# Optimization experiments

Hardware: AMD Instinct MI355X
Metric: run time of the kernel (lower is better)

The kernel has to match this reference:

```python
import jax, jax.numpy as jnp
import numpy as np

SLOPE_IN = 0.01  # F.leaky_relu default in the wrapper
SLOPE = 0.2      # DGCNN convention inside EdgeConv blocks
K = 40           # num_points -> k nearest neighbors
LOW = 16         # lowest_size: decoder starting grid
DOM = 128        # domain_size: output grid


def lrelu(x, s):
    return jnp.where(x >= 0, x, s * x)


def conv2d(x, w, b, stride, pad):
    y = jax.lax.conv_general_dilated(x, w, stride, pad,
                                     dimension_numbers=('NCHW', 'OIHW', 'NCHW'))
    return y + b[None, :, None, None]


def knn_idx(x, k):
    # x: (B,C,N) -> (B,N,k) indices of k nearest neighbors (incl. self)
    xx = jnp.sum(x * x, axis=1)                   # (B,N)
    inner = jnp.einsum('bcn,bcm->bnm', x, x)      # (B,N,N)
    neg_d = 2.0 * inner - xx[:, :, None] - xx[:, None, :]
    _, idx = jax.lax.top_k(neg_d, k)
    return idx


def graph_feature(x, idx):
    # x: (B,C,N), idx: (B,N,k) -> (B,2C,N,k): concat(neighbor - center, center)
    nbr = jax.vmap(lambda xf, i: xf[:, i])(x, idx)   # (B,C,N,k)
    ctr = jnp.broadcast_to(x[..., None], nbr.shape)
    return jnp.concatenate([nbr - ctr, ctr], axis=1)


def edge_conv(x, w, b, k):
    # dynamic graph: recompute kNN on current features
    idx = knn_idx(x, k)
    f = graph_feature(x, idx)                                      # (B,2C,N,k)
    h = jnp.einsum('oc,bcnk->bonk', w, f) + b[None, :, None, None]
    return jnp.max(lrelu(h, SLOPE), axis=-1)                       # (B,O,N)


def up2(x):
    return jnp.repeat(jnp.repeat(x, 2, axis=2), 2, axis=3)


def setup_inputs() -> dict:
    key = jax.random.key(0)
    ks = jax.random.split(key, 16)

    def w(k, shape, fan_in):
        return jax.random.normal(k, shape, jnp.float32) / np.float32(np.sqrt(fan_in))

    z = lambda n: jnp.zeros((n,), jnp.float32)
    return {
        'x':  jax.random.normal(ks[0], (2, 10, 2048), jnp.float32),
        'Wc': w(ks[1], (1, 1, 5, 3), 15),      'bc': z(1),
        'W1': w(ks[2], (64, 4), 4),            'b1': z(64),
        'W2': w(ks[3], (64, 128), 128),        'b2': z(64),
        'W3': w(ks[4], (128, 128), 128),       'b3': z(128),
        'W4': w(ks[5], (256, 256), 256),       'b4': z(256),
        'W5': w(ks[6], (1024, 512), 512),      'b5': z(1024),
        'Wfc': w(ks[7], (LOW * LOW * 64, 1024), 1024), 'bfc': z(LOW * LOW * 64),
        'Wd1': w(ks[8], (32, 64, 3, 3), 64 * 9),  'bd1': z(32),
        'Wd2': w(ks[9], (16, 32, 3, 3), 32 * 9),  'bd2': z(16),
        'Wd3': w(ks[10], (1, 16, 3, 3), 16 * 9),  'bd3': z(1),
    }


def reference(x, Wc, bc, W1, b1, W2, b2, W3, b3, W4, b4, W5, b5,
              Wfc, bfc, Wd1, bd1, Wd2, bd2, Wd3, bd3):
    # prefix: conv2d (5,3)/(5,1) + leaky_relu -> (B,1,2,N) -> point coords (B,2,N)
    h = conv2d(x[:, None, :, :], Wc, bc, (5, 1), ((0, 0), (1, 1)))
    h = lrelu(h, SLOPE_IN)[:, 0]                         # (B,2,N)
    # dynamic-graph EdgeConv stack
    x1 = edge_conv(h, W1, b1, K)                         # (B,64,N)
    x2 = edge_conv(x1, W2, b2, K)                        # (B,64,N)
    x3 = edge_conv(x2, W3, b3, K)                        # (B,128,N)
    x4 = edge_conv(x3, W4, b4, K)                        # (B,256,N)
    cat = jnp.concatenate([x1, x2, x3, x4], axis=1)      # (B,512,N)
    g = lrelu(jnp.einsum('oc,bcn->bon', W5, cat) + b5[None, :, None], SLOPE)
    g = jnp.max(g, axis=-1)                              # (B,1024) global feature
    d = lrelu(g @ Wfc.T + bfc, SLOPE).reshape(-1, 64, LOW, LOW)
    d = lrelu(conv2d(up2(d), Wd1, bd1, (1, 1), ((1, 1), (1, 1))), SLOPE)
    d = lrelu(conv2d(up2(d), Wd2, bd2, (1, 1), ((1, 1), (1, 1))), SLOPE)
    d = conv2d(up2(d), Wd3, bd3, (1, 1), ((1, 1), (1, 1)))
    return d
```

## Files before the change

kernel.cpp:

```cpp
#include <hip/hip_runtime.h>
#include <hip/hip_bf16.h>

#define N_PTS 2048
#define BATCH 2
#define KNN 40

typedef __attribute__((ext_vector_type(8))) short bf16x8;
typedef __attribute__((ext_vector_type(16))) float f32x16;

__device__ __forceinline__ float lrelu(float v, float s) {
    return v >= 0.f ? v : s * v;
}

__global__ void prefix_kernel(const float* __restrict__ x, const float* __restrict__ Wc,
                              const float* __restrict__ bc, float* __restrict__ H) {
    int t = blockIdx.x * 256 + threadIdx.x;
    if (t >= BATCH * N_PTS) return;
    int b = t >> 11, n = t & 2047;
    #pragma unroll
    for (int oh = 0; oh < 2; ++oh) {
        float acc = bc[0];
        #pragma unroll
        for (int kh = 0; kh < 5; ++kh) {
            const float* xr = x + ((size_t)b * 10 + oh * 5 + kh) * N_PTS;
            #pragma unroll
            for (int kw = 0; kw < 3; ++kw) {
                int nn = n + kw - 1;
                if (nn >= 0 && nn < N_PTS) acc += xr[nn] * Wc[kh * 3 + kw];
            }
        }
        H[(size_t)t * 2 + oh] = lrelu(acc, 0.01f);
    }
}

__global__ void xx_kernel(const float* __restrict__ X, int S, long bsX, int C,
                          float* __restrict__ XX) {
    int t = blockIdx.x * 256 + threadIdx.x;
    if (t >= BATCH * N_PTS) return;
    int b = t >> 11, n = t & 2047;
    const float* row = X + (size_t)b * bsX + (size_t)n * S;
    float s = 0.f;
    for (int c4 = 0; c4 < C; c4 += 4) {
        float4 q = *(const float4*)(row + c4);
        s += q.x * q.x;
        s += q.y * q.y;
        s += q.z * q.z;
        s += q.w * q.w;
    }
    XX[t] = s;
}

__global__ __launch_bounds__(256) void gram_small_kernel(const float* __restrict__ X, long bsX,
                                                         long nstride,
                                                         float* __restrict__ negd) {
    __shared__ float AsT[2][68];
    __shared__ float BsT[2][68];
    __shared__ float xxr[64];
    __shared__ float xxc[64];
    int bz = blockIdx.z;
    const float* Xb = X + (size_t)bz * bsX;
    float* nd = negd + (size_t)bz * nstride;
    int tid = threadIdx.x;
    int r0 = blockIdx.y * 64, c0 = blockIdx.x * 64;
    int ty = tid >> 4, tx = tid & 15;
    if (tid < 128) {
        int r = tid >> 1, c = tid & 1;
        AsT[c][r] = Xb[(size_t)(r0 + r) * 2 + c];
        BsT[c][r] = Xb[(size_t)(c0 + r) * 2 + c];
        int v = (tid < 64) ? (r0 + tid) : (c0 + tid - 64);
        float x0 = Xb[(size_t)v * 2], x1 = Xb[(size_t)v * 2 + 1];
        float s = 0.f;
        s += x0 * x0;
        s += x1 * x1;
        if (tid < 64) xxr[tid] = s; else xxc[tid - 64] = s;
    }
    __syncthreads();
    float acc[4][4] = {};
    #pragma unroll
    for (int k = 0; k < 2; ++k) {
        float4 a = *(const float4*)&AsT[k][ty * 4];
        float4 b = *(const float4*)&BsT[k][tx * 4];
        #pragma unroll
        for (int i = 0; i < 4; ++i)
            #pragma unroll
            for (int j = 0; j < 4; ++j)
                acc[i][j] += (&a.x)[i] * (&b.x)[j];
    }
    #pragma unroll
    for (int i = 0; i < 4; ++i) {
        int r = r0 + ty * 4 + i;
        float xr = xxr[ty * 4 + i];
        #pragma unroll
        for (int j = 0; j < 4; ++j) {
            int c = c0 + tx * 4 + j;
            nd[(size_t)r * N_PTS + c] = 2.0f * acc[i][j] - xr - xxc[tx * 4 + j];
        }
    }
}

template<int C>
__global__ void cvt_split_strided_kernel(const float* __restrict__ src, int S,
                                         short* __restrict__ hi, short* __restrict__ lo,
                                         int totalRows) {
    int t = blockIdx.x * 256 + threadIdx.x;
    constexpr int perRow = C / 4;
    int row = t / perRow, c4 = (t % perRow) * 4;
    if (row >= totalRows) return;
    float4 v = *(const float4*)(src + (size_t)row * S + c4);
    short4 h, l;
    #pragma unroll
    for (int j = 0; j < 4; ++j) {
        float xv = (&v.x)[j];
        __hip_bfloat16 hb = __float2bfloat16(xv);
        float hf = __bfloat162float(hb);
        __hip_bfloat16 lb = __float2bfloat16(xv - hf);
        (&h.x)[j] = *reinterpret_cast<short*>(&hb);
        (&l.x)[j] = *reinterpret_cast<short*>(&lb);
    }
    *(short4*)(hi + (size_t)row * C + c4) = h;
    *(short4*)(lo + (size_t)row * C + c4) = l;
}

template<int C, int STAGE>
__global__ __launch_bounds__(256) void gram_mfma_kernel(
        const short* __restrict__ Xh, const short* __restrict__ Xl, long bsX,
        const float* __restrict__ xx, long xxstride,
        float* __restrict__ negd, long nstride) {
    constexpr int NCH = C / 16;
    __shared__ float xr_s[128];
    __shared__ float xc_s[128];
    int bz = blockIdx.z;
    const short* Ah = Xh + (size_t)bz * bsX;
    const short* Al = Xl + (size_t)bz * bsX;
    const float* xxb = xx + (size_t)bz * xxstride;
    float* nd = negd + (size_t)bz * nstride;
    int tid = threadIdx.x;
    int wave = tid >> 6, lane = tid & 63;
    int wm = wave >> 1, wn = wave & 1;
    int r0 = blockIdx.y * 128 + wm * 64;
    int c0 = blockIdx.x * 128 + wn * 64;
    int rr = lane & 31, kg = lane >> 5;
    if (tid < 128) xr_s[tid] = xxb[blockIdx.y * 128 + tid];
    else           xc_s[tid - 128] = xxb[blockIdx.x * 128 + (tid - 128)];
    const int FS = 32 * C;
    const short* pAh = Ah + (size_t)(r0 + rr) * C + kg * 8;
    const short* pAl = Al + (size_t)(r0 + rr) * C + kg * 8;
    const short* pBh = Ah + (size_t)(c0 + rr) * C + kg * 8;
    const short* pBl = Al + (size_t)(c0 + rr) * C + kg * 8;
    f32x16 a00 = {}, a01 = {}, a10 = {}, a11 = {};
    bf16x8 ah0 = *(const bf16x8*)(pAh);
    bf16x8 ah1 = *(const bf16x8*)(pAh + FS);
    bf16x8 al0 = *(const bf16x8*)(pAl);
    bf16x8 al1 = *(const bf16x8*)(pAl + FS);
    bf16x8 bh0 = *(const bf16x8*)(pBh);
    bf16x8 bh1 = *(const bf16x8*)(pBh + FS);
    bf16x8 bl0 = *(const bf16x8*)(pBl);
    bf16x8 bl1 = *(const bf16x8*)(pBl + FS);
    #pragma unroll 2
    for (int kc = 0; kc < NCH; ++kc) {
        int kn = ((kc + 1) & (NCH - 1)) * 16;
        bf16x8 nah0 = *(const bf16x8*)(pAh + kn);
        bf16x8 nah1 = *(const bf16x8*)(pAh + kn + FS);
        bf16x8 nal0 = *(const bf16x8*)(pAl + kn);
        bf16x8 nal1 = *(const bf16x8*)(pAl + kn + FS);
        bf16x8 nbh0 = *(const bf16x8*)(pBh + kn);
        bf16x8 nbh1 = *(const bf16x8*)(pBh + kn + FS);
        bf16x8 nbl0 = *(const bf16x8*)(pBl + kn);
        bf16x8 nbl1 = *(const bf16x8*)(pBl + kn + FS);
        a00 = __builtin_amdgcn_mfma_f32_32x32x16_bf16(ah0, bh0, a00, 0, 0, 0);
        a00 = __builtin_amdgcn_mfma_f32_32x32x16_bf16(ah0, bl0, a00, 0, 0, 0);
        a00 = __builtin_amdgcn_mfma_f32_32x32x16_bf16(al0, bh0, a00, 0, 0, 0);
        a01 = __builtin_amdgcn_mfma_f32_32x32x16_bf16(ah0, bh1, a01, 0, 0, 0);
        a01 = __builtin_amdgcn_mfma_f32_32x32x16_bf16(ah0, bl1, a01, 0, 0, 0);
        a01 = __builtin_amdgcn_mfma_f32_32x32x16_bf16(al0, bh1, a01, 0, 0, 0);
        a10 = __builtin_amdgcn_mfma_f32_32x32x16_bf16(ah1, bh0, a10, 0, 0, 0);
        a10 = __builtin_amdgcn_mfma_f32_32x32x16_bf16(ah1, bl0, a10, 0, 0, 0);
        a10 = __builtin_amdgcn_mfma_f32_32x32x16_bf16(al1, bh0, a10, 0, 0, 0);
        a11 = __builtin_amdgcn_mfma_f32_32x32x16_bf16(ah1, bh1, a11, 0, 0, 0);
        a11 = __builtin_amdgcn_mfma_f32_32x32x16_bf16(ah1, bl1, a11, 0, 0, 0);
        a11 = __builtin_amdgcn_mfma_f32_32x32x16_bf16(al1, bh1, a11, 0, 0, 0);
        ah0 = nah0; ah1 = nah1; al0 = nal0; al1 = nal1;
        bh0 = nbh0; bh1 = nbh1; bl0 = nbl0; bl1 = nbl1;
    }
    __syncthreads();
    int colF = lane & 31;
    int hi4 = (lane >> 5) * 4;
    #pragma unroll
    for (int f = 0; f < 4; ++f) {
        int fm = f >> 1, fn = f & 1;
        int cIn = wn * 64 + fn * 32 + colF;
        float xc = xc_s[cIn];
        float* ndr = nd + (size_t)(blockIdx.y * 128) * N_PTS + blockIdx.x * 128 + cIn;
        #pragma unroll
        for (int reg = 0; reg < 16; ++reg) {
            float av = (f == 0) ? a00[reg] : (f == 1) ? a01[reg] : (f == 2) ? a10[reg] : a11[reg];
            int rIn = wm * 64 + fm * 32 + (reg & 3) + 8 * (reg >> 2) + hi4;
            ndr[(size_t)rIn * N_PTS] = 2.0f * av - xr_s[rIn] - xc;
        }
    }
}

template<int STAGE>
__global__ __launch_bounds__(256) void topk_kernel(const float* __restrict__ negd, long nstride,
                                                   int* __restrict__ idx_out) {
    __shared__ unsigned hist[2048];
    __shared__ unsigned cand[2048];
    __shared__ unsigned wsum[4];
    __shared__ unsigned sc[4];
    __shared__ unsigned tieb;
    int bz = blockIdx.y;
    int n = blockIdx.x;
    int tid = threadIdx.x;
    int wave = tid >> 6, lane = tid & 63;
    const float* row = negd + (size_t)bz * nstride + (size_t)n * N_PTS;
    float4 v0 = ((const float4*)row)[tid];
    float4 v1 = ((const float4*)row)[tid + 256];
    unsigned k0[4], k1[4];
    #pragma unroll
    for (int e = 0; e < 4; ++e) {
        unsigned u = __float_as_uint((&v0.x)[e]);
        k0[e] = (u & 0x80000000u) ? ~u : (u | 0x80000000u);
        u = __float_as_uint((&v1.x)[e]);
        k1[e] = (u & 0x80000000u) ? ~u : (u | 0x80000000u);
    }
    for (int i = tid; i < 2048; i += 256) hist[i] = 0u;
    if (tid == 0) { sc[2] = 0u; sc[3] = 0u; }
    __syncthreads();
    #pragma unroll
    for (int e = 0; e < 4; ++e) {
        atomicAdd(&hist[k0[e] >> 21], 1u);
        atomicAdd(&hist[k1[e] >> 21], 1u);
    }
    __syncthreads();
    unsigned r = KNN;
    {
        unsigned chunk = 0;
        #pragma unroll
        for (int q = 0; q < 8; ++q) chunk += hist[tid * 8 + q];
        unsigned s = chunk;
        #pragma unroll
        for (int off = 1; off < 64; off <<= 1) {
            unsigned v = __shfl_down(s, off);
            if (lane + off < 64) s += v;
        }
        if (lane == 0) wsum[wave] = s;
        __syncthreads();
        unsigned add = 0;
        for (int w = wave + 1; w < 4; ++w) add += wsum[w];
        unsigned St = s + add, Sn = St - chunk;
        if (St >= r && Sn < r) { sc[0] = (unsigned)tid; sc[1] = r - Sn; }
        __syncthreads();
        if (tid == 0) {
            int c = (int)sc[0]; unsigned rc = sc[1];
            unsigned cum = 0; int b = c * 8 + 7;
            for (;; --b) { cum += hist[b]; if (cum >= rc) break; }
            sc[0] = (unsigned)b; sc[1] = rc - (cum - hist[b]);
        }
        __syncthreads();
    }
    unsigned p1 = sc[0]; r = sc[1];
    __syncthreads();
    for (int i = tid; i < 2048; i += 256) hist[i] = 0u;
    __syncthreads();
    int* out = idx_out + ((size_t)bz * N_PTS + n) * KNN;
    #pragma unroll
    for (int h = 0; h < 2; ++h) {
        #pragma unroll
        for (int e = 0; e < 4; ++e) {
            unsigned u = (h == 0) ? k0[e] : k1[e];
            int j = (tid + h * 256) * 4 + e;
            unsigned b = u >> 21;
            if (b > p1) {
                out[atomicAdd(&sc[2], 1u)] = j;
            } else if (b == p1) {
                unsigned low = u & 0x1FFFFFu;
                cand[atomicAdd(&sc[3], 1u)] = (low << 11) | (unsigned)j;
                atomicAdd(&hist[low >> 10], 1u);
            }
        }
    }
    __syncthreads();
    int cnt = (int)sc[3];
    {
        unsigned chunk = 0;
        #pragma unroll
        for (int q = 0; q < 8; ++q) chunk += hist[tid * 8 + q];
        unsigned s = chunk;
        #pragma unroll
        for (int off = 1; off < 64; off <<= 1) {
            unsigned v = __shfl_down(s, off);
            if (lane + off < 64) s += v;
        }
        if (lane == 0) wsum[wave] = s;
        __syncthreads();
        unsigned add = 0;
        for (int w = wave + 1; w < 4; ++w) add += wsum[w];
        unsigned St = s + add, Sn = St - chunk;
        if (St >= r && Sn < r) { sc[0] = (unsigned)tid; sc[1] = r - Sn; }
        __syncthreads();
        if (tid == 0) {
            int c = (int)sc[0]; unsigned rc = sc[1];
            unsigned cum = 0; int b = c * 8 + 7;
            for (;; --b) { cum += hist[b]; if (cum >= rc) break; }
            sc[0] = (unsigned)b; sc[1] = rc - (cum - hist[b]);
        }
        __syncthreads();
    }
    unsigned b2 = sc[0]; r = sc[1];
    __syncthreads();
    for (int i = tid; i < 1024; i += 256) hist[i] = 0u;
    __syncthreads();
    for (int i = tid; i < cnt; i += 256) {
        unsigned p = cand[i];
        if ((p >> 21) == b2) atomicAdd(&hist[(p >> 11) & 0x3FFu], 1u);
    }
    __syncthreads();
    {
        unsigned chunk = 0;
        #pragma unroll
        for (int q = 0; q < 4; ++q) chunk += hist[tid * 4 + q];
        unsigned s = chunk;
        #pragma unroll
        for (int off = 1; off < 64; off <<= 1) {
            unsigned v = __shfl_down(s, off);
            if (lane + off < 64) s += v;
        }
        if (lane == 0) wsum[wave] = s;
        __syncthreads();
        unsigned add = 0;
        for (int w = wave + 1; w < 4; ++w) add += wsum[w];
        unsigned St = s + add, Sn = St - chunk;
        if (St >= r && Sn < r) { sc[0] = (unsigned)tid; sc[1] = r - Sn; }
        __syncthreads();
        if (tid == 0) {
            int c = (int)sc[0]; unsigned rc = sc[1];
            unsigned cum = 0; int b = c * 4 + 3;
            for (;; --b) { cum += hist[b]; if (cum >= rc) break; }
            sc[0] = (unsigned)b; sc[1] = rc - (cum - hist[b]);
        }
        __syncthreads();
    }
    unsigned Tlow = (b2 << 10) | sc[0];
    unsigned r3 = sc[1];
    __syncthreads();
    for (int i = tid; i < cnt; i += 256) {
        unsigned p = cand[i];
        if ((p >> 11) > Tlow) out[atomicAdd(&sc[2], 1u)] = (int)(p & 0x7FFu);
    }
    __syncthreads();
    int last = -1;
    for (unsigned t = 0; t < r3; ++t) {
        unsigned m = 0xFFFFFFFFu;
        for (int i = tid; i < cnt; i += 256) {
            unsigned p = cand[i];
            if ((p >> 11) == Tlow) {
                int j = (int)(p & 0x7FFu);
                if (j > last && (unsigned)j < m) m = (unsigned)j;
            }
        }
        hist[tid] = m;
        __syncthreads();
        for (int st = 128; st >= 1; st >>= 1) {
            if (tid < st) hist[tid] = min(hist[tid], hist[tid + st]);
            __syncthreads();
        }
        if (tid == 0) { out[KNN - (int)r3 + (int)t] = (int)hist[0]; tieb = hist[0]; }
        __syncthreads();
        last = (int)tieb;
    }
}

template<int C, int O, int STAGE>
__global__ __launch_bounds__(256) void ya_z_kernel(const float* __restrict__ X, int S, long bsX,
                                                   const float* __restrict__ W,
                                                   const float* __restrict__ bias,
                                                   float* __restrict__ YaT, float* __restrict__ ZT) {
    constexpr int KC = (C < 32) ? C : 32;
    __shared__ float Xs[16][KC + 1];
    __shared__ float WaS[KC][64];
    __shared__ float WbS[KC][64];
    int b = blockIdx.z;
    const float* Xb = X + (size_t)b * bsX;
    int n0 = blockIdx.x * 16, o0 = blockIdx.y * 64;
    int tid = threadIdx.x, ty = tid >> 4, tx = tid & 15;
    float aa[4] = {}, ab[4] = {};
    for (int k0 = 0; k0 < C; k0 += KC) {
        __syncthreads();
        for (int i = tid; i < 16 * KC; i += 256) {
            int rw = i / KC, c = i % KC;
            Xs[rw][c] = Xb[(size_t)(n0 + rw) * S + k0 + c];
        }
        for (int i = tid; i < 64 * KC; i += 256) {
            int rw = i / KC, c = i % KC;
            int scol = rw ^ ((c & 15) << 2);
            WaS[c][scol] = W[(size_t)(o0 + rw) * 2 * C + k0 + c];
            WbS[c][scol] = W[(size_t)(o0 + rw) * 2 * C + C + k0 + c];
        }
        __syncthreads();
        #pragma unroll
        for (int k = 0; k < KC; ++k) {
            float xv = Xs[ty][k];
            int m = (k & 15) << 2;
            float4 wa = *(const float4*)&WaS[k][(tx * 4) ^ m];
            float4 wb = *(const float4*)&WbS[k][(tx * 4) ^ m];
            #pragma unroll
            for (int j = 0; j < 4; ++j) {
                aa[j] += xv * (&wa.x)[j];
                ab[j] += xv * (&wb.x)[j];
            }
        }
    }
    int n = n0 + ty;
    float4 ya, zt;
    #pragma unroll
    for (int j = 0; j < 4; ++j) {
        int o = o0 + tx * 4 + j;
        (&ya.x)[j] = aa[j];
        (&zt.x)[j] = ab[j] - aa[j] + bias[o];
    }
    size_t off = ((size_t)b * N_PTS + n) * O + o0 + tx * 4;
    *(float4*)&YaT[off] = ya;
    *(float4*)&ZT[off] = zt;
}

template<int O, int STAGE>
__global__ __launch_bounds__(256) void edge_reduce_kernel(const float* __restrict__ YaT,
                                                          const float* __restrict__ ZT,
                                                          const int* __restrict__ IDX,
                                                          float* __restrict__ CATp, int coloff) {
    int b = blockIdx.y;
    int tid = threadIdx.x;
    int n = blockIdx.x * (256 / O) + tid / O;
    int o = tid & (O - 1);
    const float* Ya_b = YaT + (size_t)b * N_PTS * O;
    float z = ZT[((size_t)b * N_PTS + n) * O + o];
    const int* ir = IDX + ((size_t)b * N_PTS + n) * KNN;
    float acc = -3.4e38f;
    #pragma unroll 8
    for (int k = 0; k < KNN; ++k) {
        int m = ir[k];
        float v = Ya_b[(size_t)m * O + o] + z;
        acc = fmaxf(acc, lrelu(v, 0.2f));
    }
    CATp[((size_t)b * N_PTS + n) * 512 + coloff + o] = acc;
}

__global__ void cvt_split_kernel(const float* __restrict__ src, short* __restrict__ hi,
                                 short* __restrict__ lo, int total4) {
    int t = blockIdx.x * 256 + threadIdx.x;
    if (t >= total4) return;
    float4 v = ((const float4*)src)[t];
    short4 h, l;
    #pragma unroll
    for (int j = 0; j < 4; ++j) {
        float xv = (&v.x)[j];
        __hip_bfloat16 hb = __float2bfloat16(xv);
        float hf = __bfloat162float(hb);
        __hip_bfloat16 lb = __float2bfloat16(xv - hf);
        (&h.x)[j] = *reinterpret_cast<short*>(&hb);
        (&l.x)[j] = *reinterpret_cast<short*>(&lb);
    }
    ((short4*)hi)[t] = h;
    ((short4*)lo)[t] = l;
}

__global__ __launch_bounds__(256) void w5max_mfma_kernel(
        const short* __restrict__ Ah, const short* __restrict__ Al,
        const short* __restrict__ Bh, const short* __restrict__ Bl,
        const float* __restrict__ b5, float* __restrict__ PART) {
    __shared__ float red[2][128];
    int b = blockIdx.z;
    int tid = threadIdx.x;
    int wave = tid >> 6, lane = tid & 63;
    int wm = wave >> 1, wn = wave & 1;
    int m0 = blockIdx.x * 128 + wm * 64;
    int o0 = blockIdx.y * 128 + wn * 64;
    int rr = lane & 31;
    int kg = lane >> 5;
    const int FS = 32 * 512;
    const short* pAh = Ah + ((size_t)b * N_PTS + m0 + rr) * 512 + kg * 8;
    const short* pAl = Al + ((size_t)b * N_PTS + m0 + rr) * 512 + kg * 8;
    const short* pBh = Bh + (size_t)(o0 + rr) * 512 + kg * 8;
    const short* pBl = Bl + (size_t)(o0 + rr) * 512 + kg * 8;
    f32x16 a00 = {}, a01 = {}, a10 = {}, a11 = {};
    bf16x8 ah0 = *(const bf16x8*)(pAh);
    bf16x8 ah1 = *(const bf16x8*)(pAh + FS);
    bf16x8 al0 = *(const bf16x8*)(pAl);
    bf16x8 al1 = *(const bf16x8*)(pAl + FS);
    bf16x8 bh0 = *(const bf16x8*)(pBh);
    bf16x8 bh1 = *(const bf16x8*)(pBh + FS);
    bf16x8 bl0 = *(const bf16x8*)(pBl);
    bf16x8 bl1 = *(const bf16x8*)(pBl + FS);
    #pragma unroll 2
    for (int kc = 0; kc < 32; ++kc) {
        int kn = ((kc + 1) & 31) * 16;
        bf16x8 nah0 = *(const bf16x8*)(pAh + kn);
        bf16x8 nah1 = *(const bf16x8*)(pAh + kn + FS);
        bf16x8 nal0 = *(const bf16x8*)(pAl + kn);
        bf16x8 nal1 = *(const bf16x8*)(pAl + kn + FS);
        bf16x8 nbh0 = *(const bf16x8*)(pBh + kn);
        bf16x8 nbh1 = *(const bf16x8*)(pBh + kn + FS);
        bf16x8 nbl0 = *(const bf16x8*)(pBl + kn);
        bf16x8 nbl1 = *(const bf16x8*)(pBl + kn + FS);
        a00 = __builtin_amdgcn_mfma_f32_32x32x16_bf16(ah0, bh0, a00, 0, 0, 0);
        a00 = __builtin_amdgcn_mfma_f32_32x32x16_bf16(ah0, bl0, a00, 0, 0, 0);
        a00 = __builtin_amdgcn_mfma_f32_32x32x16_bf16(al0, bh0, a00, 0, 0, 0);
        a01 = __builtin_amdgcn_mfma_f32_32x32x16_bf16(ah0, bh1, a01, 0, 0, 0);
        a01 = __builtin_amdgcn_mfma_f32_32x32x16_bf16(ah0, bl1, a01, 0, 0, 0);
        a01 = __builtin_amdgcn_mfma_f32_32x32x16_bf16(al0, bh1, a01, 0, 0, 0);
        a10 = __builtin_amdgcn_mfma_f32_32x32x16_bf16(ah1, bh0, a10, 0, 0, 0);
        a10 = __builtin_amdgcn_mfma_f32_32x32x16_bf16(ah1, bl0, a10, 0, 0, 0);
        a10 = __builtin_amdgcn_mfma_f32_32x32x16_bf16(al1, bh0, a10, 0, 0, 0);
        a11 = __builtin_amdgcn_mfma_f32_32x32x16_bf16(ah1, bh1, a11, 0, 0, 0);
        a11 = __builtin_amdgcn_mfma_f32_32x32x16_bf16(ah1, bl1, a11, 0, 0, 0);
        a11 = __builtin_amdgcn_mfma_f32_32x32x16_bf16(al1, bh1, a11, 0, 0, 0);
        ah0 = nah0; ah1 = nah1; al0 = nal0; al1 = nal1;
        bh0 = nbh0; bh1 = nbh1; bl0 = nbl0; bl1 = nbl1;
    }
    #pragma unroll
    for (int fn = 0; fn < 2; ++fn) {
        float bo = b5[o0 + fn * 32 + rr];
        float m = -3.4e38f;
        #pragma unroll
        for (int r = 0; r < 16; ++r) {
            float v0 = (fn == 0) ? a00[r] : a01[r];
            float v1 = (fn == 0) ? a10[r] : a11[r];
            m = fmaxf(m, lrelu(v0 + bo, 0.2f));
            m = fmaxf(m, lrelu(v1 + bo, 0.2f));
        }
        m = fmaxf(m, __shfl_xor(m, 32));
        red[wm][wn * 64 + fn * 32 + rr] = m;
    }
    __syncthreads();
    if (tid < 128)
        PART[((size_t)b * 16 + blockIdx.x) * 1024 + blockIdx.y * 128 + tid] =
            fmaxf(red[0][tid], red[1][tid]);
}

__global__ void greduce_kernel(const float* __restrict__ PART, float* __restrict__ G) {
    int t = blockIdx.x * 256 + threadIdx.x;
    if (t >= BATCH * 1024) return;
    int b = t >> 10, o = t & 1023;
    const float* p = PART + (size_t)b * 16 * 1024 + o;
    float m = -3.4e38f;
    for (int nb = 0; nb < 16; ++nb) m = fmaxf(m, p[(size_t)nb * 1024]);
    G[t] = m;
}

__global__ __launch_bounds__(256) void fc_kernel(const float* __restrict__ G,
                                                 const float* __restrict__ Wfc,
                                                 const float* __restrict__ bfc,
                                                 float* __restrict__ D0) {
    __shared__ float gl[2][1024];
    int tid = threadIdx.x;
    for (int i = tid; i < 2048; i += 256) gl[i >> 10][i & 1023] = G[i];
    __syncthreads();
    int wave = tid >> 6, lane = tid & 63;
    int j = blockIdx.x * 4 + wave;
    const float* wr = Wfc + (size_t)j * 1024;
    float a0 = 0.f, a1 = 0.f;
    for (int i = lane; i < 1024; i += 64) {
        float w = wr[i];
        a0 += w * gl[0][i];
        a1 += w * gl[1][i];
    }
    #pragma unroll
    for (int off = 32; off; off >>= 1) { a0 += __shfl_xor(a0, off); a1 += __shfl_xor(a1, off); }
    if (lane == 0) {
        float bb = bfc[j];
        D0[j] = lrelu(a0 + bb, 0.2f);
        D0[16384 + j] = lrelu(a1 + bb, 0.2f);
    }
}

template<int CI, int CO, int HI, int WI, int RELU>
__global__ __launch_bounds__(256) void upconv_quad_kernel(const float* __restrict__ in,
                                                          const float* __restrict__ W,
                                                          const float* __restrict__ bias,
                                                          float* __restrict__ out) {
    const int qid = blockIdx.x * 256 + threadIdx.x;
    const int p = qid / WI, q = qid % WI;
    const int co = blockIdx.y, b = blockIdx.z;
    const int HO = HI * 2, WO = WI * 2;
    int off[3][3];
    float msk[3][3];
    #pragma unroll
    for (int r = 0; r < 3; ++r) {
        int pr = p - 1 + r;
        float rm = (pr >= 0 && pr < HI) ? 1.f : 0.f;
        int prc = min(max(pr, 0), HI - 1);
        #pragma unroll
        for (int c = 0; c < 3; ++c) {
            int qc = q - 1 + c;
            float cm = (qc >= 0 && qc < WI) ? 1.f : 0.f;
            int qcc = min(max(qc, 0), WI - 1);
            off[r][c] = prc * WI + qcc;
            msk[r][c] = rm * cm;
        }
    }
    const float* inb = in + (size_t)(b * CI) * HI * WI;
    const float* wco = W + (size_t)co * CI * 9;
    float bb = bias[co];
    float a00 = bb, a01 = bb, a10 = bb, a11 = bb;
    const int me[3] = {0, 1, 1}, mo[3] = {1, 1, 2};
    #pragma unroll 4
    for (int ci = 0; ci < CI; ++ci) {
        const float* ip = inb + (size_t)ci * HI * WI;
        const float* wp = wco + ci * 9;
        float v[3][3];
        #pragma unroll
        for (int r = 0; r < 3; ++r)
            #pragma unroll
            for (int c = 0; c < 3; ++c)
                v[r][c] = msk[r][c] * ip[off[r][c]];
        #pragma unroll
        for (int dy = 0; dy < 3; ++dy) {
            #pragma unroll
            for (int dx = 0; dx < 3; ++dx) {
                float w = wp[dy * 3 + dx];
                a00 += w * v[me[dy]][me[dx]];
                a01 += w * v[me[dy]][mo[dx]];
                a10 += w * v[mo[dy]][me[dx]];
                a11 += w * v[mo[dy]][mo[dx]];
            }
        }
    }
    if (RELU) {
        a00 = lrelu(a00, 0.2f); a01 = lrelu(a01, 0.2f);
        a10 = lrelu(a10, 0.2f); a11 = lrelu(a11, 0.2f);
    }
    float* ob = out + ((size_t)(b * CO + co) * HO + 2 * p) * WO + 2 * q;
    float2 r0 = {a00, a01}, r1 = {a10, a11};
    *(float2*)ob = r0;
    *(float2*)(ob + WO) = r1;
}

extern "C" void kernel_launch(void* const* d_in, const int* in_sizes, int n_in,
                              void* d_out, int out_size, void* d_ws, size_t ws_size,
                              hipStream_t stream) {
    const float* x   = (const float*)d_in[0];
    const float* Wc  = (const float*)d_in[1];
    const float* bc  = (const float*)d_in[2];
    const float* W1  = (const float*)d_in[3];
    const float* b1  = (const float*)d_in[4];
    const float* W2  = (const float*)d_in[5];
    const float* b2  = (const float*)d_in[6];
    const float* W3  = (const float*)d_in[7];
    const float* b3  = (const float*)d_in[8];
    const float* W4  = (const float*)d_in[9];
    const float* b4  = (const float*)d_in[10];
    const float* W5  = (const float*)d_in[11];
    const float* b5  = (const float*)d_in[12];
    const float* Wfc = (const float*)d_in[13];
    const float* bfc = (const float*)d_in[14];
    const float* Wd1 = (const float*)d_in[15];
    const float* bd1 = (const float*)d_in[16];
    const float* Wd2 = (const float*)d_in[17];
    const float* bd2 = (const float*)d_in[18];
    const float* Wd3 = (const float*)d_in[19];
    const float* bd3 = (const float*)d_in[20];
    float* out = (float*)d_out;

    const long NST = (long)N_PTS * N_PTS;
    const size_t TAIL_SZ = 3825664ull;
    const size_t NEED_BATCHED = 16809984ull + 33554432ull + TAIL_SZ;
    const bool batched = ws_size >= NEED_BATCHED;
    const size_t negd_bytes = batched ? 33554432ull : 16777216ull;

    char* ws = (char*)d_ws;
    float* Hb   = (float*)(ws + 0);
    float* CAT  = (float*)(ws + 32768);
    float* YaT  = (float*)(ws + 8421376);
    float* ZT   = (float*)(ws + 12615680);
    float* NEGD = (float*)(ws + 16809984);
    short* CATh = (short*)(ws + 16809984);
    short* CATl = (short*)(ws + 21004288);
    short* W5h  = (short*)(ws + 25198592);
    short* W5l  = (short*)(ws + 26247168);
    char* tail  = ws + 16809984 + negd_bytes;
    float* XX   = (float*)(tail);
    int*   IDX  = (int*)  (tail + 16384);
    float* PART = (float*)(tail + 671744);
    float* G    = (float*)(tail + 802816);
    float* D0   = (float*)(tail + 811008);
    float* DEC1 = (float*)(tail + 942080);
    float* DEC2 = (float*)(tail + 1204224);
    short* XH   = (short*)(tail + 1728512);
    short* XL   = (short*)(tail + 2777088);

    prefix_kernel<<<16, 256, 0, stream>>>(x, Wc, bc, Hb);

    if (batched) {
        gram_small_kernel<<<dim3(32, 32, 2), 256, 0, stream>>>(Hb, (long)N_PTS * 2, NST, NEGD);
        topk_kernel<1><<<dim3(N_PTS, 2), 256, 0, stream>>>(NEGD, NST, IDX);
    } else {
        for (int b = 0; b < BATCH; ++b) {
            gram_small_kernel<<<dim3(32, 32, 1), 256, 0, stream>>>(Hb + (size_t)b * N_PTS * 2, 0,
                                                                   0, NEGD);
            topk_kernel<1><<<dim3(N_PTS, 1), 256, 0, stream>>>(NEGD, 0,
                                                               IDX + (size_t)b * N_PTS * KNN);
        }
    }
    ya_z_kernel<2, 64, 1><<<dim3(128, 1, BATCH), 256, 0, stream>>>(Hb, 2, (long)N_PTS * 2,
                                                                   W1, b1, YaT, ZT);
    edge_reduce_kernel<64, 1><<<dim3(N_PTS * 64 / 256, BATCH), 256, 0, stream>>>(YaT, ZT, IDX,
                                                                                 CAT, 0);

    cvt_split_strided_kernel<64><<<(BATCH * N_PTS * 16 + 255) / 256, 256, 0, stream>>>(
        CAT + 0, 512, XH, XL, BATCH * N_PTS);
    xx_kernel<<<16, 256, 0, stream>>>(CAT + 0, 512, (long)N_PTS * 512, 64, XX);
    if (batched) {
        gram_mfma_kernel<64, 2><<<dim3(16, 16, 2), 256, 0, stream>>>(
            XH, XL, (long)N_PTS * 64, XX, N_PTS, NEGD, NST);
        topk_kernel<2><<<dim3(N_PTS, 2), 256, 0, stream>>>(NEGD, NST, IDX);
    } else {
        for (int b = 0; b < BATCH; ++b) {
            gram_mfma_kernel<64, 2><<<dim3(16, 16, 1), 256, 0, stream>>>(
                XH + (size_t)b * N_PTS * 64, XL + (size_t)b * N_PTS * 64, 0,
                XX + b * N_PTS, 0, NEGD, 0);
            topk_kernel<2><<<dim3(N_PTS, 1), 256, 0, stream>>>(NEGD, 0,
                                                               IDX + (size_t)b * N_PTS * KNN);
        }
    }
    ya_z_kernel<64, 64, 2><<<dim3(128, 1, BATCH), 256, 0, stream>>>(CAT + 0, 512,
                                                                    (long)N_PTS * 512,
                                                                    W2, b2, YaT, ZT);
    edge_reduce_kernel<64, 2><<<dim3(N_PTS * 64 / 256, BATCH), 256, 0, stream>>>(YaT, ZT, IDX,
                                                                                 CAT, 64);
    cvt_split_strided_kernel<64><<<(BATCH * N_PTS * 16 + 255) / 256, 256, 0, stream>>>(
        CAT + 64, 512, XH, XL, BATCH * N_PTS);
    xx_kernel<<<16, 256, 0, stream>>>(CAT + 64, 512, (long)N_PTS * 512, 64, XX);
    if (batched) {
        gram_mfma_kernel<64, 3><<<dim3(16, 16, 2), 256, 0, stream>>>(
            XH, XL, (long)N_PTS * 64, XX, N_PTS, NEGD, NST);
        topk_kernel<3><<<dim3(N_PTS, 2), 256, 0, stream>>>(NEGD, NST, IDX);
    } else {
        for (int b = 0; b < BATCH; ++b) {
            gram_mfma_kernel<64, 3><<<dim3(16, 16, 1), 256, 0, stream>>>(
                XH + (size_t)b * N_PTS * 64, XL + (size_t)b * N_PTS * 64, 0,
                XX + b * N_PTS, 0, NEGD, 0);
            topk_kernel<3><<<dim3(N_PTS, 1), 256, 0, stream>>>(NEGD, 0,
                                                               IDX + (size_t)b * N_PTS * KNN);
        }
    }
    ya_z_kernel<64, 128, 3><<<dim3(128, 2, BATCH), 256, 0, stream>>>(CAT + 64, 512,
                                                                     (long)N_PTS * 512,
                                                                     W3, b3, YaT, ZT);
    edge_reduce_kernel<128, 3><<<dim3(N_PTS * 128 / 256, BATCH), 256, 0, stream>>>(YaT, ZT, IDX,
                                                                                   CAT, 128);
    cvt_split_strided_kernel<128><<<(BATCH * N_PTS * 32 + 255) / 256, 256, 0, stream>>>(
        CAT + 128, 512, XH, XL, BATCH * N_PTS);
    xx_kernel<<<16, 256, 0, stream>>>(CAT + 128, 512, (long)N_PTS * 512, 128, XX);
    if (batched) {
        gram_mfma_kernel<128, 4><<<dim3(16, 16, 2), 256, 0, stream>>>(
            XH, XL, (long)N_PTS * 128, XX, N_PTS, NEGD, NST);
        topk_kernel<4><<<dim3(N_PTS, 2), 256, 0, stream>>>(NEGD, NST, IDX);
    } else {
        for (int b = 0; b < BATCH; ++b) {
            gram_mfma_kernel<128, 4><<<dim3(16, 16, 1), 256, 0, stream>>>(
                XH + (size_t)b * N_PTS * 128, XL + (size_t)b * N_PTS * 128, 0,
                XX + b * N_PTS, 0, NEGD, 0);
            topk_kernel<4><<<dim3(N_PTS, 1), 256, 0, stream>>>(NEGD, 0,
                                                               IDX + (size_t)b * N_PTS * KNN);
        }
    }
    ya_z_kernel<128, 256, 4><<<dim3(128, 4, BATCH), 256, 0, stream>>>(CAT + 128, 512,
                                                                      (long)N_PTS * 512,
                                                                      W4, b4, YaT, ZT);
    edge_reduce_kernel<256, 4><<<dim3(N_PTS * 256 / 256, BATCH), 256, 0, stream>>>(YaT, ZT, IDX,
                                                                                   CAT, 256);

    cvt_split_kernel<<<(BATCH * N_PTS * 512 / 4 + 255) / 256, 256, 0, stream>>>(
        CAT, CATh, CATl, BATCH * N_PTS * 512 / 4);
    cvt_split_kernel<<<(1024 * 512 / 4 + 255) / 256, 256, 0, stream>>>(
        W5, W5h, W5l, 1024 * 512 / 4);
    w5max_mfma_kernel<<<dim3(16, 8, BATCH), 256, 0, stream>>>(CATh, CATl, W5h, W5l, b5, PART);
    greduce_kernel<<<8, 256, 0, stream>>>(PART, G);
    fc_kernel<<<4096, 256, 0, stream>>>(G, Wfc, bfc, D0);

    upconv_quad_kernel<64, 32, 16, 16, 1><<<dim3(1, 32, BATCH), 256, 0, stream>>>(D0, Wd1, bd1,
                                                                                  DEC1);
    upconv_quad_kernel<32, 16, 32, 32, 1><<<dim3(4, 16, BATCH), 256, 0, stream>>>(DEC1, Wd2, bd2,
                                                                                  DEC2);
    upconv_quad_kernel<16, 1, 64, 64, 0><<<dim3(16, 1, BATCH), 256, 0, stream>>>(DEC2, Wd3, bd3,
                                                                                 out);
}
```

Baseline: 414.5 us.

## Fuse bf16 split conversion and squared-norm into edge reduce kernel

The edge reduce kernel now processes four output channels per thread with float4 loads. It also writes the hi/lo bf16 split of the result directly into a persistent 512-wide CATh/CATl buffer and computes per-point squared norms with a wavefront shuffle reduction. This removes the separate cvt_split_strided, xx and full-CAT cvt_split launches and their extra memory passes. The gram kernel now reads the strided CATh/CATl directly, and the workspace layout is reshuffled to keep CATh/CATl in the tail so they are not overwritten by NEGD. The costs are a larger workspace requirement and strided gram loads.

```diff
diff --git a/kernel.cpp b/kernel.cpp
--- a/kernel.cpp
+++ b/kernel.cpp
@@ -31,23 +31,6 @@
         }
         H[(size_t)t * 2 + oh] = lrelu(acc, 0.01f);
     }
-}
-
-__global__ void xx_kernel(const float* __restrict__ X, int S, long bsX, int C,
-                          float* __restrict__ XX) {
-    int t = blockIdx.x * 256 + threadIdx.x;
-    if (t >= BATCH * N_PTS) return;
-    int b = t >> 11, n = t & 2047;
-    const float* row = X + (size_t)b * bsX + (size_t)n * S;
-    float s = 0.f;
-    for (int c4 = 0; c4 < C; c4 += 4) {
-        float4 q = *(const float4*)(row + c4);
-        s += q.x * q.x;
-        s += q.y * q.y;
-        s += q.z * q.z;
-        s += q.w * q.w;
-    }
-    XX[t] = s;
 }
 
 __global__ __launch_bounds__(256) void gram_small_kernel(const float* __restrict__ X, long bsX,
@@ -98,32 +81,9 @@
     }
 }
 
-template<int C>
-__global__ void cvt_split_strided_kernel(const float* __restrict__ src, int S,
-                                         short* __restrict__ hi, short* __restrict__ lo,
-                                         int totalRows) {
-    int t = blockIdx.x * 256 + threadIdx.x;
-    constexpr int perRow = C / 4;
-    int row = t / perRow, c4 = (t % perRow) * 4;
-    if (row >= totalRows) return;
-    float4 v = *(const float4*)(src + (size_t)row * S + c4);
-    short4 h, l;
-    #pragma unroll
-    for (int j = 0; j < 4; ++j) {
-        float xv = (&v.x)[j];
-        __hip_bfloat16 hb = __float2bfloat16(xv);
-        float hf = __bfloat162float(hb);
-        __hip_bfloat16 lb = __float2bfloat16(xv - hf);
-        (&h.x)[j] = *reinterpret_cast<short*>(&hb);
-        (&l.x)[j] = *reinterpret_cast<short*>(&lb);
-    }
-    *(short4*)(hi + (size_t)row * C + c4) = h;
-    *(short4*)(lo + (size_t)row * C + c4) = l;
-}
-
 template<int C, int STAGE>
 __global__ __launch_bounds__(256) void gram_mfma_kernel(
-        const short* __restrict__ Xh, const short* __restrict__ Xl, long bsX,
+        const short* __restrict__ Xh, const short* __restrict__ Xl, long bsX, int S,
         const float* __restrict__ xx, long xxstride,
         float* __restrict__ negd, long nstride) {
     constexpr int NCH = C / 16;
@@ -142,11 +102,11 @@
     int rr = lane & 31, kg = lane >> 5;
     if (tid < 128) xr_s[tid] = xxb[blockIdx.y * 128 + tid];
     else           xc_s[tid - 128] = xxb[blockIdx.x * 128 + (tid - 128)];
-    const int FS = 32 * C;
-    const short* pAh = Ah + (size_t)(r0 + rr) * C + kg * 8;
-    const short* pAl = Al + (size_t)(r0 + rr) * C + kg * 8;
-    const short* pBh = Ah + (size_t)(c0 + rr) * C + kg * 8;
-    const short* pBl = Al + (size_t)(c0 + rr) * C + kg * 8;
+    const int FS = 32 * S;
+    const short* pAh = Ah + (size_t)(r0 + rr) * S + kg * 8;
+    const short* pAl = Al + (size_t)(r0 + rr) * S + kg * 8;
+    const short* pBh = Ah + (size_t)(c0 + rr) * S + kg * 8;
+    const short* pBl = Al + (size_t)(c0 + rr) * S + kg * 8;
     f32x16 a00 = {}, a01 = {}, a10 = {}, a11 = {};
     bf16x8 ah0 = *(const bf16x8*)(pAh);
     bf16x8 ah1 = *(const bf16x8*)(pAh + FS);
@@ -423,26 +383,53 @@
     *(float4*)&ZT[off] = zt;
 }
 
-template<int O, int STAGE>
+template<int O, int STAGE, int AUX>
 __global__ __launch_bounds__(256) void edge_reduce_kernel(const float* __restrict__ YaT,
                                                           const float* __restrict__ ZT,
                                                           const int* __restrict__ IDX,
-                                                          float* __restrict__ CATp, int coloff) {
+                                                          float* __restrict__ CATp,
+                                                          short* __restrict__ CATh,
+                                                          short* __restrict__ CATl,
+                                                          float* __restrict__ XX, int coloff) {
+    constexpr int TPR = O / 4;
     int b = blockIdx.y;
     int tid = threadIdx.x;
-    int n = blockIdx.x * (256 / O) + tid / O;
-    int o = tid & (O - 1);
+    int n = blockIdx.x * (256 / TPR) + tid / TPR;
+    int o = (tid % TPR) * 4;
     const float* Ya_b = YaT + (size_t)b * N_PTS * O;
-    float z = ZT[((size_t)b * N_PTS + n) * O + o];
-    const int* ir = IDX + ((size_t)b * N_PTS + n) * KNN;
-    float acc = -3.4e38f;
+    size_t rowoff = (size_t)b * N_PTS + n;
+    float4 z = *(const float4*)&ZT[rowoff * O + o];
+    const int* ir = IDX + rowoff * KNN;
+    float4 acc = {-3.4e38f, -3.4e38f, -3.4e38f, -3.4e38f};
     #pragma unroll 8
     for (int k = 0; k < KNN; ++k) {
         int m = ir[k];
-        float v = Ya_b[(size_t)m * O + o] + z;
-        acc = fmaxf(acc, lrelu(v, 0.2f));
-    }
-    CATp[((size_t)b * N_PTS + n) * 512 + coloff + o] = acc;
+        float4 v = *(const float4*)&Ya_b[(size_t)m * O + o];
+        acc.x = fmaxf(acc.x, lrelu(v.x + z.x, 0.2f));
+        acc.y = fmaxf(acc.y, lrelu(v.y + z.y, 0.2f));
+        acc.z = fmaxf(acc.z, lrelu(v.z + z.z, 0.2f));
+        acc.w = fmaxf(acc.w, lrelu(v.w + z.w, 0.2f));
+    }
+    size_t coff = rowoff * 512 + coloff + o;
+    *(float4*)&CATp[coff] = acc;
+    short4 h, l;
+    #pragma unroll
+    for (int j = 0; j < 4; ++j) {
+        float xv = (&acc.x)[j];
+        __hip_bfloat16 hb = __float2bfloat16(xv);
+        float hf = __bfloat162float(hb);
+        __hip_bfloat16 lb = __float2bfloat16(xv - hf);
+        (&h.x)[j] = *reinterpret_cast<short*>(&hb);
+        (&l.x)[j] = *reinterpret_cast<short*>(&lb);
+    }
+    *(short4*)&CATh[coff] = h;
+    *(short4*)&CATl[coff] = l;
+    if (AUX) {
+        float sq = acc.x * acc.x + acc.y * acc.y + acc.z * acc.z + acc.w * acc.w;
+        #pragma unroll
+        for (int off = 1; off < TPR; off <<= 1) sq += __shfl_xor(sq, off);
+        if ((tid % TPR) == 0) XX[rowoff] = sq;
+    }
 }
 
 __global__ void cvt_split_kernel(const float* __restrict__ src, short* __restrict__ hi,
@@ -662,7 +649,7 @@
     float* out = (float*)d_out;
 
     const long NST = (long)N_PTS * N_PTS;
-    const size_t TAIL_SZ = 3825664ull;
+    const size_t TAIL_SZ = 12214272ull;
     const size_t NEED_BATCHED = 16809984ull + 33554432ull + TAIL_SZ;
     const bool batched = ws_size >= NEED_BATCHED;
     const size_t negd_bytes = batched ? 33554432ull : 16777216ull;
@@ -673,10 +660,6 @@
     float* YaT  = (float*)(ws + 8421376);
     float* ZT   = (float*)(ws + 12615680);
     float* NEGD = (float*)(ws + 16809984);
-    short* CATh = (short*)(ws + 16809984);
-    short* CATl = (short*)(ws + 21004288);
-    short* W5h  = (short*)(ws + 25198592);
-    short* W5l  = (short*)(ws + 26247168);
     char* tail  = ws + 16809984 + negd_bytes;
     float* XX   = (float*)(tail);
     int*   IDX  = (int*)  (tail + 16384);
@@ -685,8 +668,10 @@
     float* D0   = (float*)(tail + 811008);
     float* DEC1 = (float*)(tail + 942080);
     float* DEC2 = (float*)(tail + 1204224);
-    short* XH   = (short*)(tail + 1728512);
-    short* XL   = (short*)(tail + 2777088);
+    short* W5h  = (short*)(tail + 1728512);
+    short* W5l  = (short*)(tail + 2777088);
+    short* CATh = (short*)(tail + 3825664);
+    short* CATl = (short*)(tail + 8019968);
 
     prefix_kernel<<<16, 256, 0, stream>>>(x, Wc, bc, Hb);
 
@@ -703,20 +688,17 @@
     }
     ya_z_kernel<2, 64, 1><<<dim3(128, 1, BATCH), 256, 0, stream>>>(Hb, 2, (long)N_PTS * 2,
                                                                    W1, b1, YaT, ZT);
-    edge_reduce_kernel<64, 1><<<dim3(N_PTS * 64 / 256, BATCH), 256, 0, stream>>>(YaT, ZT, IDX,
-                                                                                 CAT, 0);
-
-    cvt_split_strided_kernel<64><<<(BATCH * N_PTS * 16 + 255) / 256, 256, 0, stream>>>(
-        CAT + 0, 512, XH, XL, BATCH * N_PTS);
-    xx_kernel<<<16, 256, 0, stream>>>(CAT + 0, 512, (long)N_PTS * 512, 64, XX);
+    edge_reduce_kernel<64, 1, 1><<<dim3(128, BATCH), 256, 0, stream>>>(YaT, ZT, IDX, CAT,
+                                                                       CATh, CATl, XX, 0);
+
     if (batched) {
         gram_mfma_kernel<64, 2><<<dim3(16, 16, 2), 256, 0, stream>>>(
-            XH, XL, (long)N_PTS * 64, XX, N_PTS, NEGD, NST);
+            CATh + 0, CATl + 0, (long)N_PTS * 512, 512, XX, N_PTS, NEGD, NST);
         topk_kernel<2><<<dim3(N_PTS, 2), 256, 0, stream>>>(NEGD, NST, IDX);
     } else {
         for (int b = 0; b < BATCH; ++b) {
             gram_mfma_kernel<64, 2><<<dim3(16, 16, 1), 256, 0, stream>>>(
-                XH + (size_t)b * N_PTS * 64, XL + (size_t)b * N_PTS * 64, 0,
+                CATh + 0 + (size_t)b * N_PTS * 512, CATl + 0 + (size_t)b * N_PTS * 512, 0, 512,
                 XX + b * N_PTS, 0, NEGD, 0);
             topk_kernel<2><<<dim3(N_PTS, 1), 256, 0, stream>>>(NEGD, 0,
                                                                IDX + (size_t)b * N_PTS * KNN);
@@ -725,19 +707,17 @@
     ya_z_kernel<64, 64, 2><<<dim3(128, 1, BATCH), 256, 0, stream>>>(CAT + 0, 512,
                                                                     (long)N_PTS * 512,
                                                                     W2, b2, YaT, ZT);
-    edge_reduce_kernel<64, 2><<<dim3(N_PTS * 64 / 256, BATCH), 256, 0, stream>>>(YaT, ZT, IDX,
-                                                                                 CAT, 64);
-    cvt_split_strided_kernel<64><<<(BATCH * N_PTS * 16 + 255) / 256, 256, 0, stream>>>(
-        CAT + 64, 512, XH, XL, BATCH * N_PTS);
-    xx_kernel<<<16, 256, 0, stream>>>(CAT + 64, 512, (long)N_PTS * 512, 64, XX);
+    edge_reduce_kernel<64, 2, 1><<<dim3(128, BATCH), 256, 0, stream>>>(YaT, ZT, IDX, CAT,
+                                                                       CATh, CATl, XX, 64);
+
     if (batched) {
         gram_mfma_kernel<64, 3><<<dim3(16, 16, 2), 256, 0, stream>>>(
-            XH, XL, (long)N_PTS * 64, XX, N_PTS, NEGD, NST);
+            CATh + 64, CATl + 64, (long)N_PTS * 512, 512, XX, N_PTS, NEGD, NST);
         topk_kernel<3><<<dim3(N_PTS, 2), 256, 0, stream>>>(NEGD, NST, IDX);
     } else {
         for (int b = 0; b < BATCH; ++b) {
             gram_mfma_kernel<64, 3><<<dim3(16, 16, 1), 256, 0, stream>>>(
-                XH + (size_t)b * N_PTS * 64, XL + (size_t)b * N_PTS * 64, 0,
+                CATh + 64 + (size_t)b * N_PTS * 512, CATl + 64 + (size_t)b * N_PTS * 512, 0, 512,
                 XX + b * N_PTS, 0, NEGD, 0);
             topk_kernel<3><<<dim3(N_PTS, 1), 256, 0, stream>>>(NEGD, 0,
                                                                IDX + (size_t)b * N_PTS * KNN);
@@ -746,19 +726,17 @@
     ya_z_kernel<64, 128, 3><<<dim3(128, 2, BATCH), 256, 0, stream>>>(CAT + 64, 512,
                                                                      (long)N_PTS * 512,
                                                                      W3, b3, YaT, ZT);
-    edge_reduce_kernel<128, 3><<<dim3(N_PTS * 128 / 256, BATCH), 256, 0, stream>>>(YaT, ZT, IDX,
-                                                                                   CAT, 128);
-    cvt_split_strided_kernel<128><<<(BATCH * N_PTS * 32 + 255) / 256, 256, 0, stream>>>(
-        CAT + 128, 512, XH, XL, BATCH * N_PTS);
-    xx_kernel<<<16, 256, 0, stream>>>(CAT + 128, 512, (long)N_PTS * 512, 128, XX);
+    edge_reduce_kernel<128, 3, 1><<<dim3(256, BATCH), 256, 0, stream>>>(YaT, ZT, IDX, CAT,
+                                                                        CATh, CATl, XX, 128);
+
     if (batched) {
         gram_mfma_kernel<128, 4><<<dim3(16, 16, 2), 256, 0, stream>>>(
-            XH, XL, (long)N_PTS * 128, XX, N_PTS, NEGD, NST);
+            CATh + 128, CATl + 128, (long)N_PTS * 512, 512, XX, N_PTS, NEGD, NST);
         topk_kernel<4><<<dim3(N_PTS, 2), 256, 0, stream>>>(NEGD, NST, IDX);
     } else {
         for (int b = 0; b < BATCH; ++b) {
             gram_mfma_kernel<128, 4><<<dim3(16, 16, 1), 256, 0, stream>>>(
-                XH + (size_t)b * N_PTS * 128, XL + (size_t)b * N_PTS * 128, 0,
+                CATh + 128 + (size_t)b * N_PTS * 512, CATl + 128 + (size_t)b * N_PTS * 512, 0, 512,
                 XX + b * N_PTS, 0, NEGD, 0);
             topk_kernel<4><<<dim3(N_PTS, 1), 256, 0, stream>>>(NEGD, 0,
                                                                IDX + (size_t)b * N_PTS * KNN);
@@ -767,11 +745,9 @@
     ya_z_kernel<128, 256, 4><<<dim3(128, 4, BATCH), 256, 0, stream>>>(CAT + 128, 512,
                                                                       (long)N_PTS * 512,
                                                                       W4, b4, YaT, ZT);
-    edge_reduce_kernel<256, 4><<<dim3(N_PTS * 256 / 256, BATCH), 256, 0, stream>>>(YaT, ZT, IDX,
-                                                                                   CAT, 256);
-
-    cvt_split_kernel<<<(BATCH * N_PTS * 512 / 4 + 255) / 256, 256, 0, stream>>>(
-        CAT, CATh, CATl, BATCH * N_PTS * 512 / 4);
+    edge_reduce_kernel<256, 4, 0><<<dim3(512, BATCH), 256, 0, stream>>>(YaT, ZT, IDX, CAT,
+                                                                        CATh, CATl, XX, 256);
+
     cvt_split_kernel<<<(1024 * 512 / 4 + 255) / 256, 256, 0, stream>>>(
         W5, W5h, W5l, 1024 * 512 / 4);
     w5max_mfma_kernel<<<dim3(16, 8, BATCH), 256, 0, stream>>>(CATh, CATl, W5h, W5l, b5, PART);
```

Result: faster. 347.0 us (median of 2 runs) (-16.3%).
